# Optimization experiments

Hardware: AMD Instinct MI355X
Metric: run time of the kernel (lower is better)

## Reference

```python
import jax, jax.numpy as jnp
import numpy as np

H = 128
NH = 8
HD = H // NH  # 16
TANH_ALPHA = 10.0
LN_EPS = 1e-5


def _layer_norm(x, g, b):
    mu = jnp.mean(x, axis=-1, keepdims=True)
    var = jnp.mean((x - mu) ** 2, axis=-1, keepdims=True)
    return (x - mu) / jnp.sqrt(var + LN_EPS) * g + b


def setup_inputs() -> dict:
    key = jax.random.key(0)
    ks = jax.random.split(key, 24)
    B, N = 1024, 500

    def p(k, shape):
        return jax.random.normal(k, shape, dtype=jnp.float32) * 0.05

    inp = {
        "node_embeddings": jax.random.normal(ks[0], (B, N, H), jnp.float32),
        "graph_embeddings": jax.random.normal(ks[1], (B, H), jnp.float32),
        "first_node": jax.random.randint(ks[2], (B,), 0, N, jnp.int32),
        "current_node": jax.random.randint(ks[3], (B,), 0, N, jnp.int32),
        "mask": jax.random.randint(ks[4], (B, N), 0, 2, jnp.int32),
        # linear_first: Linear(384, 128)
        "W_first": p(ks[5], (H, 3 * H)),
        "b_first": p(ks[6], (H,)),
        # ln1 / ln2
        "g1": jnp.ones((H,), jnp.float32),
        "beta1": jnp.zeros((H,), jnp.float32),
        "g2": jnp.ones((H,), jnp.float32),
        "beta2": jnp.zeros((H,), jnp.float32),
        # LSTM(128,128) single layer, gate order i,f,g,o
        "W_ih": p(ks[7], (4 * H, H)),
        "W_hh": p(ks[8], (4 * H, H)),
        "b_ih": p(ks[9], (4 * H,)),
        "b_hh": p(ks[10], (4 * H,)),
        # attention / output projections (no bias)
        "Wq": p(ks[11], (H, H)),
        "Wk": p(ks[12], (H, H)),
        "Wv": p(ks[13], (H, H)),
        "Wproj": p(ks[14], (H, H)),
        # logitk: Linear(128,128) with bias
        "Wlk": p(ks[15], (H, H)),
        "blk": p(ks[16], (H,)),
    }
    return inp


def reference(node_embeddings, graph_embeddings, W_first, b_first, g1, beta1,
              W_ih, W_hh, b_ih, b_hh, g2, beta2, Wq, Wk, Wv, Wproj, Wlk, blk,
              first_node, current_node, mask):
    B, N, _ = node_embeddings.shape
    dt = node_embeddings.dtype

    # build_cache: K/V/logitK projections of all node embeddings
    ck = node_embeddings @ Wk.T                # [B,N,128]
    cv = node_embeddings @ Wv.T                # [B,N,128]
    lk = node_embeddings @ Wlk.T + blk         # [B,N,128]

    # context construction
    bidx = jnp.arange(B)
    first_emb = node_embeddings[bidx, first_node]    # [B,128]
    cur_emb = node_embeddings[bidx, current_node]    # [B,128]
    context = jnp.concatenate([graph_embeddings, first_emb, cur_emb], axis=1)
    context = _layer_norm(context @ W_first.T + b_first, g1, beta1)

    # single LSTM step from zero state (build_cache resets h,c to 0)
    gates = context @ W_ih.T + b_ih + b_hh           # h_prev = 0 -> no W_hh term
    i, f, g, o = jnp.split(gates, 4, axis=-1)
    c = jax.nn.sigmoid(i) * jnp.tanh(g)              # c_prev = 0
    h = jax.nn.sigmoid(o) * jnp.tanh(c)
    ctx = _layer_norm(h, g2, beta2)

    # multi-head single-query attention; note (e h) split: head is the FAST dim
    q = (ctx @ Wq.T).reshape(B, HD, NH).transpose(0, 2, 1)       # [B,h,e]
    k = ck.reshape(B, N, HD, NH).transpose(0, 3, 1, 2)           # [B,h,N,e]
    v = cv.reshape(B, N, HD, NH).transpose(0, 3, 1, 2)           # [B,h,N,e]
    maskf = mask.astype(dt)
    scores = jnp.einsum('bhe,bhne->bhn', q, k) / np.sqrt(HD) + maskf[:, None, :]
    att = jax.nn.softmax(scores, axis=-1)
    oh = jnp.einsum('bhn,bhne->bhe', att, v)                     # [B,h,e]
    att_out = oh.reshape(B, H)                                   # (h e): h slow, e fast

    context_emb = att_out @ Wproj.T                              # [B,128]
    comp = jnp.einsum('be,bne->bn', lk, context_emb[:, None, :].squeeze(1)[:, :][None].squeeze(0) if False else context_emb) if False else jnp.einsum('bne,be->bn', lk, context_emb)
    comp = comp / np.sqrt(H)
    comp = TANH_ALPHA * jnp.tanh(comp)
    out = jnp.where(mask == 1, -jnp.inf, comp)
    return out
```

## Files before the change

kernel.cpp:

```cpp
#include <hip/hip_runtime.h>
#include <math.h>

#define NBATCH 1024
#define NNODE  500
#define HDIM   128
#define NHEAD  8
#define G1K    4
#define RSQRT_H 0.08838834764831845f
#define MASK_NEG (-1e30f)

typedef __attribute__((ext_vector_type(8))) short  short8;
typedef __attribute__((ext_vector_type(4))) float  f32x4;

__device__ __forceinline__ short bftr(float f) {
    return (short)(__float_as_uint(f) >> 16);
}

template<int G>
__device__ __forceinline__ void block_ln(float (&x)[G], const float* __restrict__ gw,
                                         const float* __restrict__ bw,
                                         int t, int lane, int wv, float (*wpart)[G])
{
    float s[G];
    #pragma unroll
    for (int g = 0; g < G; ++g) s[g] = x[g];
    #pragma unroll
    for (int off = 32; off >= 1; off >>= 1) {
        #pragma unroll
        for (int g = 0; g < G; ++g) s[g] += __shfl_xor(s[g], off, 64);
    }
    if (lane == 0) {
        #pragma unroll
        for (int g = 0; g < G; ++g) wpart[wv][g] = s[g];
    }
    __syncthreads();
    float mu[G];
    #pragma unroll
    for (int g = 0; g < G; ++g) mu[g] = (wpart[0][g] + wpart[1][g]) * (1.f/128.f);
    __syncthreads();
    #pragma unroll
    for (int g = 0; g < G; ++g) { float d = x[g] - mu[g]; s[g] = d * d; }
    #pragma unroll
    for (int off = 32; off >= 1; off >>= 1) {
        #pragma unroll
        for (int g = 0; g < G; ++g) s[g] += __shfl_xor(s[g], off, 64);
    }
    if (lane == 0) {
        #pragma unroll
        for (int g = 0; g < G; ++g) wpart[wv][g] = s[g];
    }
    __syncthreads();
    float gv = gw[t], bv = bw[t];
    #pragma unroll
    for (int g = 0; g < G; ++g) {
        float var = (wpart[0][g] + wpart[1][g]) * (1.f/128.f);
        x[g] = (x[g] - mu[g]) / sqrtf(var + 1e-5f) * gv + bv;
    }
    __syncthreads();
}

__global__ __launch_bounds__(128) void k1_context(
    const float* __restrict__ node, const float* __restrict__ graph,
    const int* __restrict__ firstn, const int* __restrict__ curn,
    const float* __restrict__ W_first, const float* __restrict__ b_first,
    const float* __restrict__ g1, const float* __restrict__ beta1,
    const float* __restrict__ W_ih, const float* __restrict__ b_ih,
    const float* __restrict__ b_hh, const float* __restrict__ g2,
    const float* __restrict__ beta2, const float* __restrict__ Wq,
    const float* __restrict__ Wk, float* __restrict__ qW_out)
{
    const int t = threadIdx.x;
    const int lane = t & 63, wv = t >> 6;
    const int b0 = blockIdx.x * G1K;
    __shared__ __align__(16) float ctx[G1K][384];
    __shared__ __align__(16) float bufB[G1K][128];
    __shared__ float wpart[2][G1K];

    #pragma unroll
    for (int g = 0; g < G1K; ++g) {
        int b = b0 + g;
        ctx[g][t]       = graph[b*HDIM + t];
        ctx[g][128 + t] = node[((size_t)b*NNODE + firstn[b])*HDIM + t];
        ctx[g][256 + t] = node[((size_t)b*NNODE + curn[b])*HDIM + t];
    }
    __syncthreads();

    float x[G1K];
    {
        const float4* Wf4 = (const float4*)W_first;
        float bf = b_first[t];
        #pragma unroll
        for (int g = 0; g < G1K; ++g) x[g] = bf;
        for (int j4 = 0; j4 < 96; ++j4) {
            float4 w = Wf4[t*96 + j4];
            #pragma unroll
            for (int g = 0; g < G1K; ++g) {
                float4 c = ((const float4*)ctx[g])[j4];
                x[g] += c.x*w.x + c.y*w.y + c.z*w.z + c.w*w.w;
            }
        }
    }
    block_ln<G1K>(x, g1, beta1, t, lane, wv, wpart);

    #pragma unroll
    for (int g = 0; g < G1K; ++g) bufB[g][t] = x[g];
    __syncthreads();

    float gi[G1K], gg[G1K], go[G1K];
    {
        const float4* Wih4 = (const float4*)W_ih;
        float bi = b_ih[t]       + b_hh[t];
        float bg = b_ih[256 + t] + b_hh[256 + t];
        float bo = b_ih[384 + t] + b_hh[384 + t];
        #pragma unroll
        for (int g = 0; g < G1K; ++g) { gi[g] = bi; gg[g] = bg; go[g] = bo; }
        for (int j4 = 0; j4 < 32; ++j4) {
            float4 wi = Wih4[(size_t)t*32 + j4];
            float4 wg = Wih4[(size_t)(256 + t)*32 + j4];
            float4 wo = Wih4[(size_t)(384 + t)*32 + j4];
            #pragma unroll
            for (int g = 0; g < G1K; ++g) {
                float4 v = ((const float4*)bufB[g])[j4];
                gi[g] += v.x*wi.x + v.y*wi.y + v.z*wi.z + v.w*wi.w;
                gg[g] += v.x*wg.x + v.y*wg.y + v.z*wg.z + v.w*wg.w;
                go[g] += v.x*wo.x + v.y*wo.y + v.z*wo.z + v.w*wo.w;
            }
        }
    }
    #pragma unroll
    for (int g = 0; g < G1K; ++g) {
        float ig = 1.f / (1.f + expf(-gi[g]));
        float cc = ig * tanhf(gg[g]);
        float og = 1.f / (1.f + expf(-go[g]));
        x[g] = og * tanhf(cc);
    }
    block_ln<G1K>(x, g2, beta2, t, lane, wv, wpart);

    #pragma unroll
    for (int g = 0; g < G1K; ++g) bufB[g][t] = x[g];
    __syncthreads();

    float q8[G1K];
    #pragma unroll
    for (int g = 0; g < G1K; ++g) q8[g] = 0.f;
    {
        const float4* Wq4 = (const float4*)Wq;
        for (int j4 = 0; j4 < 32; ++j4) {
            float4 w = Wq4[t*32 + j4];
            #pragma unroll
            for (int g = 0; g < G1K; ++g) {
                float4 v = ((const float4*)bufB[g])[j4];
                q8[g] += v.x*w.x + v.y*w.y + v.z*w.z + v.w*w.w;
            }
        }
    }
    __syncthreads();
    #pragma unroll
    for (int g = 0; g < G1K; ++g) bufB[g][t] = q8[g];
    __syncthreads();

    for (int h = 0; h < NHEAD; ++h) {
        float a[G1K];
        #pragma unroll
        for (int g = 0; g < G1K; ++g) a[g] = 0.f;
        for (int e = 0; e < 16; ++e) {
            float w = Wk[(e*8 + h)*HDIM + t];
            #pragma unroll
            for (int g = 0; g < G1K; ++g) a[g] += bufB[g][e*8 + h] * w;
        }
        #pragma unroll
        for (int g = 0; g < G1K; ++g)
            qW_out[((size_t)(b0 + g)*NHEAD + h)*HDIM + t] = 0.25f * a[g];
    }
}

__global__ __launch_bounds__(256) void k2_fused(
    const float* __restrict__ node, const int* __restrict__ mask,
    const float* __restrict__ qW, const float* __restrict__ Wv,
    const float* __restrict__ Wproj, const float* __restrict__ Wlk,
    const float* __restrict__ blk_, float* __restrict__ wce_out,
    float* __restrict__ bias_out)
{
    const int b = blockIdx.x, tid = threadIdx.x;
    const int lane = tid & 63, w = tid >> 6;

    __shared__ __align__(16) float s_p[NNODE*NHEAD];
    __shared__ float s_red[4][8];
    __shared__ float s_m[8], s_l[8];
    __shared__ __align__(16) float s_an[NHEAD*HDIM];
    __shared__ __align__(16) float s_ao[HDIM], s_ce[HDIM];
    __shared__ __align__(16) float s_part[8][HDIM];

    const float* nodeb = node + (size_t)b*NNODE*HDIM;

    {
        const int h = lane & 15;
        const bool hok = (h < NHEAD);
        const int koff = (lane >> 4) << 3;

        short8 bfr[4];
        {
            const float* qrow = qW + ((size_t)b*NHEAD + (hok ? h : 0))*HDIM;
            #pragma unroll
            for (int kk = 0; kk < 4; ++kk) {
                short8 f = (short8)0;
                if (hok) {
                    const int c0 = kk*32 + koff;
                    float4 w0 = *(const float4*)(qrow + c0);
                    float4 w1 = *(const float4*)(qrow + c0 + 4);
                    f[0]=bftr(w0.x); f[1]=bftr(w0.y); f[2]=bftr(w0.z); f[3]=bftr(w0.w);
                    f[4]=bftr(w1.x); f[5]=bftr(w1.y); f[6]=bftr(w1.z); f[7]=bftr(w1.w);
                }
                bfr[kk] = f;
            }
        }
        #pragma unroll
        for (int it = 0; it < 8; ++it) {
            const int rowbase = it*64 + w*16;
            const int arow = rowbase + (lane & 15);
            const bool rok = (arow < NNODE);
            const float* nrow = nodeb + (size_t)arow*HDIM;
            f32x4 acc = {0.f, 0.f, 0.f, 0.f};
            #pragma unroll
            for (int kk = 0; kk < 4; ++kk) {
                const int c0 = kk*32 + koff;
                short8 afr = (short8)0;
                if (rok) {
                    float4 v0 = *(const float4*)(nrow + c0);
                    float4 v1 = *(const float4*)(nrow + c0 + 4);
                    afr[0]=bftr(v0.x); afr[1]=bftr(v0.y); afr[2]=bftr(v0.z); afr[3]=bftr(v0.w);
                    afr[4]=bftr(v1.x); afr[5]=bftr(v1.y); afr[6]=bftr(v1.z); afr[7]=bftr(v1.w);
                }
                acc = __builtin_amdgcn_mfma_f32_16x16x32_bf16(afr, bfr[kk], acc, 0, 0, 0);
            }
            if (hok) {
                #pragma unroll
                for (int j = 0; j < 4; ++j) {
                    int r = rowbase + ((lane >> 4) << 2) + j;
                    if (r < NNODE) s_p[r*NHEAD + h] = acc[j];
                }
            }
        }
    }
    __syncthreads();

    const int* maskb = mask + (size_t)b*NNODE;
    {
        float mx[8];
        #pragma unroll
        for (int h = 0; h < 8; ++h) mx[h] = -INFINITY;
        for (int r = tid; r < NNODE; r += 256) {
            float mf = (float)maskb[r];
            #pragma unroll
            for (int h = 0; h < 8; ++h) {
                float v = s_p[r*8 + h] + mf;
                s_p[r*8 + h] = v;
                mx[h] = fmaxf(mx[h], v);
            }
        }
        #pragma unroll
        for (int off = 1; off <= 32; off <<= 1) {
            #pragma unroll
            for (int h = 0; h < 8; ++h) mx[h] = fmaxf(mx[h], __shfl_xor(mx[h], off, 64));
        }
        if (lane == 0) {
            #pragma unroll
            for (int h = 0; h < 8; ++h) s_red[w][h] = mx[h];
        }
        __syncthreads();
        if (tid < 8)
            s_m[tid] = fmaxf(fmaxf(s_red[0][tid], s_red[1][tid]),
                             fmaxf(s_red[2][tid], s_red[3][tid]));
        __syncthreads();
        float ls[8];
        #pragma unroll
        for (int h = 0; h < 8; ++h) ls[h] = 0.f;
        for (int r = tid; r < NNODE; r += 256) {
            #pragma unroll
            for (int h = 0; h < 8; ++h) {
                float p = __expf(s_p[r*8 + h] - s_m[h]);
                s_p[r*8 + h] = p;
                ls[h] += p;
            }
        }
        #pragma unroll
        for (int off = 1; off <= 32; off <<= 1) {
            #pragma unroll
            for (int h = 0; h < 8; ++h) ls[h] += __shfl_xor(ls[h], off, 64);
        }
        if (lane == 0) {
            #pragma unroll
            for (int h = 0; h < 8; ++h) s_red[w][h] = ls[h];
        }
        __syncthreads();
        if (tid < 8)
            s_l[tid] = s_red[0][tid] + s_red[1][tid] + s_red[2][tid] + s_red[3][tid];
        __syncthreads();
    }

    {
        const int h2 = tid >> 5, d8 = tid & 31;
        f32x4 acc = {0.f, 0.f, 0.f, 0.f};
        const float4* nb = (const float4*)nodeb + d8;
        #pragma unroll 4
        for (int n = 0; n < NNODE; ++n) {
            float4 v = nb[(size_t)n*32];
            float p = s_p[n*8 + h2];
            acc[0] += p*v.x; acc[1] += p*v.y; acc[2] += p*v.z; acc[3] += p*v.w;
        }
        float inv = 1.f / s_l[h2];
        float4 o = make_float4(acc[0]*inv, acc[1]*inv, acc[2]*inv, acc[3]*inv);
        *(float4*)(s_an + h2*HDIM + d8*4) = o;
    }
    __syncthreads();

    {
        const int c = tid >> 1, half = tid & 1;
        const int h = c >> 4, e = c & 15, row = e*8 + h;
        const float4* wr = (const float4*)(Wv + (size_t)row*HDIM) + half*16;
        const float4* ar = (const float4*)(s_an + h*HDIM) + half*16;
        float sum = 0.f;
        #pragma unroll
        for (int j = 0; j < 16; ++j) {
            float4 wv4 = wr[j], av = ar[j];
            sum += av.x*wv4.x + av.y*wv4.y + av.z*wv4.z + av.w*wv4.w;
        }
        sum += __shfl_xor(sum, 1, 64);
        if (half == 0) s_ao[c] = sum;
    }
    __syncthreads();
    {
        const int c = tid >> 1, half = tid & 1;
        const float4* wr = (const float4*)(Wproj + (size_t)c*HDIM) + half*16;
        const float4* ar = (const float4*)s_ao + half*16;
        float sum = 0.f;
        #pragma unroll
        for (int j = 0; j < 16; ++j) {
            float4 wv4 = wr[j], av = ar[j];
            sum += av.x*wv4.x + av.y*wv4.y + av.z*wv4.z + av.w*wv4.w;
        }
        sum += __shfl_xor(sum, 1, 64);
        if (half == 0) s_ce[c] = sum;
    }
    __syncthreads();
    {
        const int cg = tid >> 5, dq = tid & 31;
        float4 part = make_float4(0.f, 0.f, 0.f, 0.f);
        #pragma unroll
        for (int i = 0; i < 16; ++i) {
            int c = cg*16 + i;
            float v = s_ce[c];
            float4 wv4 = ((const float4*)(Wlk + (size_t)c*HDIM))[dq];
            part.x += v*wv4.x; part.y += v*wv4.y;
            part.z += v*wv4.z; part.w += v*wv4.w;
        }
        *(float4*)(s_part[cg] + dq*4) = part;
    }
    __syncthreads();
    if (tid < 32) {
        float4 tot = make_float4(0.f, 0.f, 0.f, 0.f);
        #pragma unroll
        for (int cg = 0; cg < 8; ++cg) {
            float4 v = *(float4*)(s_part[cg] + tid*4);
            tot.x += v.x; tot.y += v.y; tot.z += v.z; tot.w += v.w;
        }
        tot.x *= RSQRT_H; tot.y *= RSQRT_H; tot.z *= RSQRT_H; tot.w *= RSQRT_H;
        *(float4*)(wce_out + (size_t)b*HDIM + tid*4) = tot;
    }
    else if (tid >= 64 && tid < 128) {
        int c = tid - 64;
        float v = s_ce[c]*blk_[c] + s_ce[c+64]*blk_[c+64];
        #pragma unroll
        for (int off = 1; off <= 32; off <<= 1) v += __shfl_xor(v, off, 64);
        if (c == 0) bias_out[b] = v * RSQRT_H;
    }
}

__global__ __launch_bounds__(256) void k3_out(
    const float* __restrict__ node, const int* __restrict__ mask,
    const float* __restrict__ wce, const float* __restrict__ biasv,
    float* __restrict__ out)
{
    const int slot = (int)((blockIdx.x*256u + threadIdx.x) >> 5);
    const int q = threadIdx.x & 31;
    const int b = slot / NNODE;
    const float4 nv = *(const float4*)(node + (size_t)slot*HDIM + q*4);
    const float4 wv = *(const float4*)(wce + (size_t)b*HDIM + q*4);
    float p = nv.x*wv.x + nv.y*wv.y + nv.z*wv.z + nv.w*wv.w;
    #pragma unroll
    for (int off = 16; off >= 1; off >>= 1) p += __shfl_xor(p, off, 32);
    if (q == 0) {
        float v = 10.f * tanhf(p + biasv[b]);
        out[slot] = (mask[slot] == 1) ? MASK_NEG : v;
    }
}

extern "C" void kernel_launch(void* const* d_in, const int* in_sizes, int n_in,
                              void* d_out, int out_size, void* d_ws, size_t ws_size,
                              hipStream_t stream) {
    const float* node    = (const float*)d_in[0];
    const float* graph   = (const float*)d_in[1];
    const int*   firstn  = (const int*)d_in[2];
    const int*   curn    = (const int*)d_in[3];
    const int*   mask    = (const int*)d_in[4];
    const float* W_first = (const float*)d_in[5];
    const float* b_first = (const float*)d_in[6];
    const float* g1      = (const float*)d_in[7];
    const float* beta1   = (const float*)d_in[8];
    const float* g2      = (const float*)d_in[9];
    const float* beta2   = (const float*)d_in[10];
    const float* W_ih    = (const float*)d_in[11];
    const float* b_ih    = (const float*)d_in[13];
    const float* b_hh    = (const float*)d_in[14];
    const float* Wq      = (const float*)d_in[15];
    const float* Wk      = (const float*)d_in[16];
    const float* Wv      = (const float*)d_in[17];
    const float* Wproj   = (const float*)d_in[18];
    const float* Wlk     = (const float*)d_in[19];
    const float* blk     = (const float*)d_in[20];
    float* out = (float*)d_out;

    float* qW    = (float*)d_ws;
    float* wce   = qW + (size_t)NBATCH*NHEAD*HDIM;
    float* biasv = wce + (size_t)NBATCH*HDIM;

    k1_context<<<NBATCH/G1K, 128, 0, stream>>>(node, graph, firstn, curn,
        W_first, b_first, g1, beta1, W_ih, b_ih, b_hh, g2, beta2, Wq, Wk, qW);
    k2_fused<<<NBATCH, 256, 0, stream>>>(node, mask, qW, Wv, Wproj, Wlk, blk,
        wce, biasv);
    k3_out<<<(NBATCH*NNODE)/8, 256, 0, stream>>>(node, mask, wce, biasv, out);
}
```

Measured before the change: 225.7 us.

## Double-buffer node loads in score MFMA loop and transpose score layout

The score phase now prefetches node rows for the next two iterations into register buffers, so global loads overlap with the bf16 conversion and MFMA work. The shared score array is switched from node-major to head-major, which changes the bank access pattern in the softmax and weighted-sum loops. The kernel also requests an occupancy hint of 4 blocks per CU and unrolls the value accumulation loop further. These changes raise register pressure, which the occupancy hint may force into spills.

After: 220.8 us. 2.2% less time.

```diff
diff --git a/kernel.cpp b/kernel.cpp
--- a/kernel.cpp
+++ b/kernel.cpp
@@ -174,7 +174,7 @@
     }
 }
 
-__global__ __launch_bounds__(256) void k2_fused(
+__global__ __launch_bounds__(256, 4) void k2_fused(
     const float* __restrict__ node, const int* __restrict__ mask,
     const float* __restrict__ qW, const float* __restrict__ Wv,
     const float* __restrict__ Wproj, const float* __restrict__ Wlk,
@@ -183,8 +183,12 @@
 {
     const int b = blockIdx.x, tid = threadIdx.x;
     const int lane = tid & 63, w = tid >> 6;
-
-    __shared__ __align__(16) float s_p[NNODE*NHEAD];
+    const int h = lane & 15;
+    const bool hok = (h < NHEAD);
+    const int g16 = lane >> 4;
+    const int koff = g16 << 3;
+
+    __shared__ __align__(16) float s_p[NHEAD*NNODE];
     __shared__ float s_red[4][8];
     __shared__ float s_m[8], s_l[8];
     __shared__ __align__(16) float s_an[NHEAD*HDIM];
@@ -194,10 +198,6 @@
     const float* nodeb = node + (size_t)b*NNODE*HDIM;
 
     {
-        const int h = lane & 15;
-        const bool hok = (h < NHEAD);
-        const int koff = (lane >> 4) << 3;
-
         short8 bfr[4];
         {
             const float* qrow = qW + ((size_t)b*NHEAD + (hok ? h : 0))*HDIM;
@@ -205,41 +205,56 @@
             for (int kk = 0; kk < 4; ++kk) {
                 short8 f = (short8)0;
                 if (hok) {
-                    const int c0 = kk*32 + koff;
-                    float4 w0 = *(const float4*)(qrow + c0);
-                    float4 w1 = *(const float4*)(qrow + c0 + 4);
+                    float4 w0 = *(const float4*)(qrow + kk*32 + koff);
+                    float4 w1 = *(const float4*)(qrow + kk*32 + koff + 4);
                     f[0]=bftr(w0.x); f[1]=bftr(w0.y); f[2]=bftr(w0.z); f[3]=bftr(w0.w);
                     f[4]=bftr(w1.x); f[5]=bftr(w1.y); f[6]=bftr(w1.z); f[7]=bftr(w1.w);
                 }
                 bfr[kk] = f;
             }
         }
-        #pragma unroll
-        for (int it = 0; it < 8; ++it) {
-            const int rowbase = it*64 + w*16;
-            const int arow = rowbase + (lane & 15);
-            const bool rok = (arow < NNODE);
-            const float* nrow = nodeb + (size_t)arow*HDIM;
+
+        float4 Ra[8], Rb[8];
+        auto loadit = [&](float4* R, int it) {
+            const int rl = it*64 + w*16 + (lane & 15);
+            if (rl < NNODE) {
+                const float* nrow = nodeb + (size_t)rl*HDIM;
+                #pragma unroll
+                for (int kk = 0; kk < 4; ++kk) {
+                    R[kk*2]   = *(const float4*)(nrow + kk*32 + koff);
+                    R[kk*2+1] = *(const float4*)(nrow + kk*32 + koff + 4);
+                }
+            } else {
+                #pragma unroll
+                for (int i = 0; i < 8; ++i) R[i] = make_float4(0.f,0.f,0.f,0.f);
+            }
+        };
+        auto computeit = [&](const float4* R, int it) {
             f32x4 acc = {0.f, 0.f, 0.f, 0.f};
             #pragma unroll
             for (int kk = 0; kk < 4; ++kk) {
-                const int c0 = kk*32 + koff;
-                short8 afr = (short8)0;
-                if (rok) {
-                    float4 v0 = *(const float4*)(nrow + c0);
-                    float4 v1 = *(const float4*)(nrow + c0 + 4);
-                    afr[0]=bftr(v0.x); afr[1]=bftr(v0.y); afr[2]=bftr(v0.z); afr[3]=bftr(v0.w);
-                    afr[4]=bftr(v1.x); afr[5]=bftr(v1.y); afr[6]=bftr(v1.z); afr[7]=bftr(v1.w);
-                }
+                float4 v0 = R[kk*2], v1 = R[kk*2+1];
+                short8 afr;
+                afr[0]=bftr(v0.x); afr[1]=bftr(v0.y); afr[2]=bftr(v0.z); afr[3]=bftr(v0.w);
+                afr[4]=bftr(v1.x); afr[5]=bftr(v1.y); afr[6]=bftr(v1.z); afr[7]=bftr(v1.w);
                 acc = __builtin_amdgcn_mfma_f32_16x16x32_bf16(afr, bfr[kk], acc, 0, 0, 0);
             }
             if (hok) {
                 #pragma unroll
                 for (int j = 0; j < 4; ++j) {
-                    int r = rowbase + ((lane >> 4) << 2) + j;
-                    if (r < NNODE) s_p[r*NHEAD + h] = acc[j];
+                    int r = it*64 + w*16 + g16*4 + j;
+                    if (r < NNODE) s_p[h*NNODE + r] = acc[j];
                 }
             }
+        };
+
+        loadit(Ra, 0);
+        loadit(Rb, 1);
+        #pragma unroll
+        for (int it = 0; it < 8; ++it) {
+            float4* cur = (it & 1) ? Rb : Ra;
+            computeit(cur, it);
+            if (it + 2 < 8) loadit(cur, it + 2);
         }
     }
     __syncthreads();
@@ -248,24 +263,24 @@
     {
         float mx[8];
         #pragma unroll
-        for (int h = 0; h < 8; ++h) mx[h] = -INFINITY;
+        for (int hh = 0; hh < 8; ++hh) mx[hh] = -INFINITY;
         for (int r = tid; r < NNODE; r += 256) {
             float mf = (float)maskb[r];
             #pragma unroll
-            for (int h = 0; h < 8; ++h) {
-                float v = s_p[r*8 + h] + mf;
-                s_p[r*8 + h] = v;
-                mx[h] = fmaxf(mx[h], v);
+            for (int hh = 0; hh < 8; ++hh) {
+                float v = s_p[hh*NNODE + r] + mf;
+                s_p[hh*NNODE + r] = v;
+                mx[hh] = fmaxf(mx[hh], v);
             }
         }
         #pragma unroll
         for (int off = 1; off <= 32; off <<= 1) {
             #pragma unroll
-            for (int h = 0; h < 8; ++h) mx[h] = fmaxf(mx[h], __shfl_xor(mx[h], off, 64));
+            for (int hh = 0; hh < 8; ++hh) mx[hh] = fmaxf(mx[hh], __shfl_xor(mx[hh], off, 64));
         }
         if (lane == 0) {
             #pragma unroll
-            for (int h = 0; h < 8; ++h) s_red[w][h] = mx[h];
+            for (int hh = 0; hh < 8; ++hh) s_red[w][hh] = mx[hh];
         }
         __syncthreads();
         if (tid < 8)
@@ -274,23 +289,23 @@
         __syncthreads();
         float ls[8];
         #pragma unroll
-        for (int h = 0; h < 8; ++h) ls[h] = 0.f;
+        for (int hh = 0; hh < 8; ++hh) ls[hh] = 0.f;
         for (int r = tid; r < NNODE; r += 256) {
             #pragma unroll
-            for (int h = 0; h < 8; ++h) {
-                float p = __expf(s_p[r*8 + h] - s_m[h]);
-                s_p[r*8 + h] = p;
-                ls[h] += p;
+            for (int hh = 0; hh < 8; ++hh) {
+                float p = __expf(s_p[hh*NNODE + r] - s_m[hh]);
+                s_p[hh*NNODE + r] = p;
+                ls[hh] += p;
             }
         }
         #pragma unroll
         for (int off = 1; off <= 32; off <<= 1) {
             #pragma unroll
-            for (int h = 0; h < 8; ++h) ls[h] += __shfl_xor(ls[h], off, 64);
+            for (int hh = 0; hh < 8; ++hh) ls[hh] += __shfl_xor(ls[hh], off, 64);
         }
         if (lane == 0) {
             #pragma unroll
-            for (int h = 0; h < 8; ++h) s_red[w][h] = ls[h];
+            for (int hh = 0; hh < 8; ++hh) s_red[w][hh] = ls[hh];
         }
         __syncthreads();
         if (tid < 8)
@@ -301,11 +316,12 @@
     {
         const int h2 = tid >> 5, d8 = tid & 31;
         f32x4 acc = {0.f, 0.f, 0.f, 0.f};
-        const float4* nb = (const float4*)nodeb + d8;
-        #pragma unroll 4
+        const float4* nb4 = (const float4*)nodeb + d8;
+        const float* prow = s_p + h2*NNODE;
+        #pragma unroll 10
         for (int n = 0; n < NNODE; ++n) {
-            float4 v = nb[(size_t)n*32];
-            float p = s_p[n*8 + h2];
+            float4 v = nb4[(size_t)n*32];
+            float p = prow[n];
             acc[0] += p*v.x; acc[1] += p*v.y; acc[2] += p*v.z; acc[3] += p*v.w;
         }
         float inv = 1.f / s_l[h2];
@@ -316,9 +332,9 @@
 
     {
         const int c = tid >> 1, half = tid & 1;
-        const int h = c >> 4, e = c & 15, row = e*8 + h;
+        const int hh = c >> 4, e = c & 15, row = e*8 + hh;
         const float4* wr = (const float4*)(Wv + (size_t)row*HDIM) + half*16;
-        const float4* ar = (const float4*)(s_an + h*HDIM) + half*16;
+        const float4* ar = (const float4*)(s_an + hh*HDIM) + half*16;
         float sum = 0.f;
         #pragma unroll
         for (int j = 0; j < 16; ++j) {
```
